# Performance work log

Measured on AMD Instinct MI355X. Metric: run time of the kernel, lower is better.

The kernel has to match this reference:

```python
import jax, jax.numpy as jnp
import numpy as np

ORDER = 24
N_POINTS = 524288


def setup_inputs() -> dict:
    key = jax.random.key(0)
    k1, k2 = jax.random.split(key)
    xyz = jax.random.uniform(k1, (N_POINTS, 3), dtype=jnp.float32)
    coeffs = jax.random.normal(k2, (ORDER ** 3,), dtype=jnp.float32) * 0.1
    return {"xyz": xyz, "coeffs": coeffs}


def reference(xyz, coeffs):
    # Faithful to: sum_{i,j,k} c[i,j,k] * sin(2pi i x) * sin(2pi j y) * sin(2pi k z)
    # but with per-axis sin tables computed once (O(order) transcendentals per point)
    # and the triple sum expressed as chained contractions (GEMM-like).
    order = ORDER
    C = coeffs.reshape(order, order, order)  # c[i,j,k]
    n = jnp.arange(order, dtype=xyz.dtype)   # frequencies 0..order-1 (i=0 row is all zeros)
    two_pi = jnp.asarray(2.0 * np.pi, dtype=xyz.dtype)
    S = jnp.sin(two_pi * xyz[:, :, None] * n)  # [N, 3, order]
    Sx, Sy, Sz = S[:, 0, :], S[:, 1, :], S[:, 2, :]  # each [N, order]
    A = jnp.einsum('nk,ijk->nij', Sz, C)   # [N, order, order]
    B = jnp.einsum('nj,nij->ni', Sy, A)    # [N, order]
    return jnp.einsum('ni,ni->n', Sx, B)   # [N]
```

## Files before the change

kernel.cpp:

```cpp
#include <hip/hip_runtime.h>

typedef _Float16 f16x2 __attribute__((ext_vector_type(2)));
typedef _Float16 f16x8 __attribute__((ext_vector_type(8)));
typedef __fp16   fp16v2 __attribute__((ext_vector_type(2)));
typedef float    f32x4 __attribute__((ext_vector_type(4)));

#define TSTRIDE 21

__global__ __launch_bounds__(256) void prep_B(const float* __restrict__ coeffs,
                                              f16x8* __restrict__ wsB)
{
    int chunk = blockIdx.x * 256 + threadIdx.x;
    int f  = chunk / 48, sl = chunk % 48;
    int s  = f >> 1,  tt = f & 1;
    int gg = sl >> 4, cc = sl & 15;
    int i  = 16 * tt + cc;
    f16x8 v;
    if (i < 24) {
        const float* src = coeffs + i * 576 + s * 24 + gg * 8;
#pragma unroll
        for (int e = 0; e < 8; ++e) v[e] = (_Float16)src[e];
    } else {
#pragma unroll
        for (int e = 0; e < 8; ++e) v[e] = (_Float16)0.f;
    }
    wsB[chunk] = v;
}

__global__ __launch_bounds__(512, 8) void fourier_main(
    const float* __restrict__ xyz,
    const f16x8* __restrict__ wsB,
    float* __restrict__ out)
{
    __shared__ __align__(16) f16x8 Bl[2304];

    const int tid  = threadIdx.x;
    const int wave = tid >> 6;
    const int lane = tid & 63;
    const int g    = lane >> 4;
    const int c    = lane & 15;

#pragma unroll
    for (int pass = 0; pass < 4; ++pass)
        Bl[pass * 512 + tid] = wsB[pass * 512 + tid];
    if (tid < 256) Bl[2048 + tid] = wsB[2048 + tid];

    const int p0 = (blockIdx.x * 8 + wave) * 32;

    float syp[2], syc[2], c2y[2];
    f16x2 sz2[2][4];
    const float kmask = (g < 3) ? 1.0f : 0.0f;

#pragma unroll
    for (int m = 0; m < 2; ++m) {
        int p = p0 + 16 * m + c;
        float y = xyz[3 * p + 1];
        float z = xyz[3 * p + 2];
        float sy1 = __builtin_amdgcn_sinf(y);
        float cy1 = __builtin_amdgcn_cosf(y);
        syp[m] = 0.f; syc[m] = sy1; c2y[m] = 2.f * cy1;
        float sz1 = __builtin_amdgcn_sinf(z);
        float cz1 = __builtin_amdgcn_cosf(z);
        float wv  = __builtin_amdgcn_fractf((float)(8 * g) * z);
        float sb  = __builtin_amdgcn_sinf(wv) * kmask;
        float cb  = __builtin_amdgcn_cosf(wv);
        float c2z = 2.f * cz1;
        float szf[8];
        szf[0] = sb;
        szf[1] = fmaf(sb, cz1, cb * sz1 * kmask);
#pragma unroll
        for (int e = 2; e < 8; ++e) szf[e] = fmaf(c2z, szf[e - 1], -szf[e - 2]);
#pragma unroll
        for (int q = 0; q < 4; ++q)
            sz2[m][q] = f16x2{(_Float16)szf[2 * q], (_Float16)szf[2 * q + 1]};
    }

    f32x4 acc[2][2] = {};

    __syncthreads();

    const int bslot = (lane < 48) ? lane : 47;
#pragma unroll
    for (int s = 1; s < 24; ++s) {
        f16x8 b0 = Bl[(2 * s + 0) * 48 + bslot];
        f16x8 b1 = Bl[(2 * s + 1) * 48 + bslot];
#pragma unroll
        for (int m = 0; m < 2; ++m) {
            _Float16 hy = (_Float16)syc[m];
            f16x2 hy2 = {hy, hy};
            f16x8 a;
#pragma unroll
            for (int q = 0; q < 4; ++q) {
                f16x2 pr = hy2 * sz2[m][q];
                a[2 * q]     = pr[0];
                a[2 * q + 1] = pr[1];
            }
            acc[m][0] = __builtin_amdgcn_mfma_f32_16x16x32_f16(a, b0, acc[m][0], 0, 0, 0);
            acc[m][1] = __builtin_amdgcn_mfma_f32_16x16x32_f16(a, b1, acc[m][1], 0, 0, 0);
            float nxt = fmaf(c2y[m], syc[m], -syp[m]);
            syp[m] = syc[m]; syc[m] = nxt;
        }
    }

    __syncthreads();

    unsigned int* Tw = (unsigned int*)Bl + wave * (32 * TSTRIDE);
#pragma unroll
    for (int m = 0; m < 2; ++m)
#pragma unroll
        for (int r = 0; r < 4; ++r) {
            int lr = 16 * m + 4 * g + r;
            fp16v2 pk = __builtin_amdgcn_cvt_pkrtz(acc[m][0][r], acc[m][1][r]);
            Tw[lr * TSTRIDE + c] = __builtin_bit_cast(unsigned int, pk);
        }

    __syncthreads();

    {
        int lr = lane & 31;
        int p  = p0 + lr;
        float x   = xyz[3 * p];
        float s1  = __builtin_amdgcn_sinf(x);
        float c1  = __builtin_amdgcn_cosf(x);
        float f16x_ = __builtin_amdgcn_fractf(16.f * x);
        float s16 = __builtin_amdgcn_sinf(f16x_);
        float c16 = __builtin_amdgcn_cosf(f16x_);
        const float c2x = 2.f * c1;
        float sA0 = 0.f,  sA1 = s1;
        float sB0 = s16,  sB1 = fmaf(s16, c1, c16 * s1);
        float res = 0.f;
        const unsigned int* Tr = Tw + lr * TSTRIDE;
#pragma unroll
        for (int w = 0; w < 16; ++w) {
            f16x2 h = __builtin_bit_cast(f16x2, Tr[w]);
            res = fmaf(sA0, (float)h[0], res);
            res = fmaf(sB0, (float)h[1], res);
            float nA = fmaf(c2x, sA1, -sA0);
            float nB = fmaf(c2x, sB1, -sB0);
            sA0 = sA1; sA1 = nA;
            sB0 = sB1; sB1 = nB;
        }
        if (lane < 32) out[p] = res;
    }
}

extern "C" void kernel_launch(void* const* d_in, const int* in_sizes, int n_in,
                              void* d_out, int out_size, void* d_ws, size_t ws_size,
                              hipStream_t stream) {
    const float* xyz    = (const float*)d_in[0];
    const float* coeffs = (const float*)d_in[1];
    float* out = (float*)d_out;
    f16x8* wsB = (f16x8*)d_ws;

    prep_B<<<9, 256, 0, stream>>>(coeffs, wsB);

    const int n = in_sizes[0] / 3;
    const int grid = n / 256;
    fourier_main<<<grid, 512, 0, stream>>>(xyz, wsB, out);
}
```

Before: 34.78 us.

## Process 64 points per wave to amortize B loads and use all lanes

Each wave now handles 64 points instead of 32, so every shared-memory B fragment load feeds four MFMA row-tiles instead of two, and the final x-contraction stage uses all 64 lanes rather than half. The grid is halved, so the per-block cost of copying the coefficient table into shared memory is spread over twice as many points. Packing now uses the cvt_pkrtz intrinsic, the x load is hoisted to the start, and the transpose stride is changed to fit the larger tile. In exchange, register pressure rises and occupancy is reduced (launch bounds drop to 4 blocks per SM).

```diff
diff --git a/kernel.cpp b/kernel.cpp
--- a/kernel.cpp
+++ b/kernel.cpp
@@ -4,8 +4,14 @@
 typedef _Float16 f16x8 __attribute__((ext_vector_type(8)));
 typedef __fp16   fp16v2 __attribute__((ext_vector_type(2)));
 typedef float    f32x4 __attribute__((ext_vector_type(4)));
+typedef unsigned int u32x4 __attribute__((ext_vector_type(4)));
 
-#define TSTRIDE 21
+#define TSTRIDE 17
+
+__device__ __forceinline__ f16x2 pk2(float lo, float hi) {
+    fp16v2 p = __builtin_amdgcn_cvt_pkrtz(lo, hi);
+    return __builtin_bit_cast(f16x2, p);
+}
 
 __global__ __launch_bounds__(256) void prep_B(const float* __restrict__ coeffs,
                                               f16x8* __restrict__ wsB)
@@ -27,7 +33,7 @@
     wsB[chunk] = v;
 }
 
-__global__ __launch_bounds__(512, 8) void fourier_main(
+__global__ __launch_bounds__(512, 4) void fourier_main(
     const float* __restrict__ xyz,
     const f16x8* __restrict__ wsB,
     float* __restrict__ out)
@@ -45,14 +51,16 @@
         Bl[pass * 512 + tid] = wsB[pass * 512 + tid];
     if (tid < 256) Bl[2048 + tid] = wsB[2048 + tid];
 
-    const int p0 = (blockIdx.x * 8 + wave) * 32;
+    const int p0 = (blockIdx.x * 8 + wave) * 64;
 
-    float syp[2], syc[2], c2y[2];
-    f16x2 sz2[2][4];
+    const float xv = xyz[3 * (p0 + lane)];
+
+    float syp[4], syc[4], c2y[4];
+    f16x2 sz2[4][4];
     const float kmask = (g < 3) ? 1.0f : 0.0f;
 
 #pragma unroll
-    for (int m = 0; m < 2; ++m) {
+    for (int m = 0; m < 4; ++m) {
         int p = p0 + 16 * m + c;
         float y = xyz[3 * p + 1];
         float z = xyz[3 * p + 2];
@@ -71,11 +79,10 @@
 #pragma unroll
         for (int e = 2; e < 8; ++e) szf[e] = fmaf(c2z, szf[e - 1], -szf[e - 2]);
 #pragma unroll
-        for (int q = 0; q < 4; ++q)
-            sz2[m][q] = f16x2{(_Float16)szf[2 * q], (_Float16)szf[2 * q + 1]};
+        for (int q = 0; q < 4; ++q) sz2[m][q] = pk2(szf[2 * q], szf[2 * q + 1]);
     }
 
-    f32x4 acc[2][2] = {};
+    f32x4 acc[4][2] = {};
 
     __syncthreads();
 
@@ -85,16 +92,15 @@
         f16x8 b0 = Bl[(2 * s + 0) * 48 + bslot];
         f16x8 b1 = Bl[(2 * s + 1) * 48 + bslot];
 #pragma unroll
-        for (int m = 0; m < 2; ++m) {
-            _Float16 hy = (_Float16)syc[m];
-            f16x2 hy2 = {hy, hy};
-            f16x8 a;
+        for (int m = 0; m < 4; ++m) {
+            f16x2 hy2 = pk2(syc[m], syc[m]);
+            u32x4 aw;
 #pragma unroll
             for (int q = 0; q < 4; ++q) {
                 f16x2 pr = hy2 * sz2[m][q];
-                a[2 * q]     = pr[0];
-                a[2 * q + 1] = pr[1];
+                aw[q] = __builtin_bit_cast(unsigned int, pr);
             }
+            f16x8 a = __builtin_bit_cast(f16x8, aw);
             acc[m][0] = __builtin_amdgcn_mfma_f32_16x16x32_f16(a, b0, acc[m][0], 0, 0, 0);
             acc[m][1] = __builtin_amdgcn_mfma_f32_16x16x32_f16(a, b1, acc[m][1], 0, 0, 0);
             float nxt = fmaf(c2y[m], syc[m], -syp[m]);
@@ -104,9 +110,9 @@
 
     __syncthreads();
 
-    unsigned int* Tw = (unsigned int*)Bl + wave * (32 * TSTRIDE);
+    unsigned int* Tw = (unsigned int*)Bl + wave * (64 * TSTRIDE);
 #pragma unroll
-    for (int m = 0; m < 2; ++m)
+    for (int m = 0; m < 4; ++m)
 #pragma unroll
         for (int r = 0; r < 4; ++r) {
             int lr = 16 * m + 4 * g + r;
@@ -117,19 +123,17 @@
     __syncthreads();
 
     {
-        int lr = lane & 31;
-        int p  = p0 + lr;
-        float x   = xyz[3 * p];
-        float s1  = __builtin_amdgcn_sinf(x);
-        float c1  = __builtin_amdgcn_cosf(x);
-        float f16x_ = __builtin_amdgcn_fractf(16.f * x);
-        float s16 = __builtin_amdgcn_sinf(f16x_);
-        float c16 = __builtin_amdgcn_cosf(f16x_);
+        int p = p0 + lane;
+        float s1  = __builtin_amdgcn_sinf(xv);
+        float c1  = __builtin_amdgcn_cosf(xv);
+        float w16 = __builtin_amdgcn_fractf(16.f * xv);
+        float s16 = __builtin_amdgcn_sinf(w16);
+        float c16 = __builtin_amdgcn_cosf(w16);
         const float c2x = 2.f * c1;
         float sA0 = 0.f,  sA1 = s1;
         float sB0 = s16,  sB1 = fmaf(s16, c1, c16 * s1);
         float res = 0.f;
-        const unsigned int* Tr = Tw + lr * TSTRIDE;
+        const unsigned int* Tr = Tw + lane * TSTRIDE;
 #pragma unroll
         for (int w = 0; w < 16; ++w) {
             f16x2 h = __builtin_bit_cast(f16x2, Tr[w]);
@@ -140,7 +144,7 @@
             sA0 = sA1; sA1 = nA;
             sB0 = sB1; sB1 = nB;
         }
-        if (lane < 32) out[p] = res;
+        out[p] = res;
     }
 }
 
@@ -155,6 +159,6 @@
     prep_B<<<9, 256, 0, stream>>>(coeffs, wsB);
 
     const int n = in_sizes[0] / 3;
-    const int grid = n / 256;
+    const int grid = n / 512;
     fourier_main<<<grid, 512, 0, stream>>>(xyz, wsB, out);
 }
```

Result: faster. 31.45 us (-9.6%).
